# Kernel optimization log

Hardware: AMD Instinct MI355X
Metric: run time of the kernel (lower is better)

Reference implementation:

```python
import jax, jax.numpy as jnp
import numpy as np

N = 20000
E = 320000
NEG_SLOPE = 0.2
LN_EPS = 1e-5


def gat_conv(x, W, a_src, a_dst, b, src, dst, heads, ch, concat):
    # x: [N, F_in]; W: [F_in, H*C]; a_src/a_dst: [H, C]; b: [H*C] or [C]
    xl = (x @ W).reshape(N, heads, ch)                      # [N,H,C]
    alpha_src = jnp.sum(xl * a_src, axis=-1)                # [N,H]
    alpha_dst = jnp.sum(xl * a_dst, axis=-1)                # [N,H]
    e = alpha_src[src] + alpha_dst[dst]                     # [E',H]
    e = jax.nn.leaky_relu(e, NEG_SLOPE)
    # segment softmax over incoming edges of each dst node
    m = jax.ops.segment_max(e, dst, num_segments=N)         # [N,H]
    m = jnp.where(jnp.isfinite(m), m, 0.0)
    ex = jnp.exp(e - m[dst])
    denom = jax.ops.segment_sum(ex, dst, num_segments=N)    # [N,H]
    alpha = ex / (denom[dst] + 1e-16)                       # [E',H]
    msg = alpha[:, :, None] * xl[src]                       # [E',H,C]
    out = jax.ops.segment_sum(msg, dst, num_segments=N)     # [N,H,C]
    if concat:
        return out.reshape(N, heads * ch) + b
    return out.mean(axis=1) + b


def layer_norm(x, g, b):
    mu = jnp.mean(x, axis=-1, keepdims=True)
    var = jnp.mean(jnp.square(x - mu), axis=-1, keepdims=True)
    return (x - mu) * jax.lax.rsqrt(var + LN_EPS) * g + b


def setup_inputs() -> dict:
    key = jax.random.key(0)
    ks = jax.random.split(key, 24)
    d = {}
    d["x"] = jax.random.normal(ks[0], (N, 50), dtype=jnp.float32)
    d["edge_index"] = jax.random.randint(ks[1], (2, E), 0, N, dtype=jnp.int64)

    def glorot(k, shape):
        fan = shape[0] + shape[-1]
        return jax.random.normal(k, shape, dtype=jnp.float32) * np.sqrt(2.0 / fan)

    # conv1: 50 -> 256, heads=4, concat
    d["W1"] = glorot(ks[2], (50, 4 * 256))
    d["a_src1"] = glorot(ks[3], (4, 256))
    d["a_dst1"] = glorot(ks[4], (4, 256))
    d["b1"] = jnp.zeros((4 * 256,), jnp.float32)
    # conv2: 1024 -> 256, heads=4, concat
    d["W2"] = glorot(ks[5], (1024, 4 * 256))
    d["a_src2"] = glorot(ks[6], (4, 256))
    d["a_dst2"] = glorot(ks[7], (4, 256))
    d["b2"] = jnp.zeros((4 * 256,), jnp.float32)
    # conv3: 1024 -> 121, heads=6, concat=False
    d["W3"] = glorot(ks[8], (1024, 6 * 121))
    d["a_src3"] = glorot(ks[9], (6, 121))
    d["a_dst3"] = glorot(ks[10], (6, 121))
    d["b3"] = jnp.zeros((121,), jnp.float32)
    # skips
    d["skipW1"] = glorot(ks[11], (50, 1024))
    d["skipb1"] = jnp.zeros((1024,), jnp.float32)
    d["skipW2"] = glorot(ks[12], (1024, 1024))
    d["skipb2"] = jnp.zeros((1024,), jnp.float32)
    # layer norms
    d["g1"] = jnp.ones((1024,), jnp.float32)
    d["beta1"] = jnp.zeros((1024,), jnp.float32)
    d["g2"] = jnp.ones((1024,), jnp.float32)
    d["beta2"] = jnp.zeros((1024,), jnp.float32)
    return d


def reference(x, edge_index, W1, a_src1, a_dst1, b1, W2, a_src2, a_dst2, b2,
              W3, a_src3, a_dst3, b3, skipW1, skipb1, skipW2, skipb2,
              g1, beta1, g2, beta2):
    # add self loops (PyG GATConv default)
    loop = jnp.arange(N, dtype=edge_index.dtype)
    src = jnp.concatenate([edge_index[0], loop])
    dst = jnp.concatenate([edge_index[1], loop])

    h = gat_conv(x, W1, a_src1, a_dst1, b1, src, dst, 4, 256, True)
    h = jax.nn.elu(layer_norm(h + (x @ skipW1 + skipb1), g1, beta1))
    h2 = gat_conv(h, W2, a_src2, a_dst2, b2, src, dst, 4, 256, True)
    h2 = jax.nn.elu(layer_norm(h2 + (h @ skipW2 + skipb2), g2, beta2))
    out = gat_conv(h2, W3, a_src3, a_dst3, b3, src, dst, 6, 121, False)
    return out
```

## Files before the change

kernel.cpp:

```cpp
#include <hip/hip_runtime.h>
#include <hip/hip_bf16.h>
#include <math.h>

typedef __attribute__((ext_vector_type(8))) __bf16 bf16x8;
typedef __attribute__((ext_vector_type(4))) float f32x4;

#if __has_builtin(__builtin_amdgcn_global_load_lds)
#define GLD16(g, l)                                                                      \
    __builtin_amdgcn_global_load_lds(                                                    \
        (const __attribute__((address_space(1))) unsigned int*)(g),                      \
        (__attribute__((address_space(3))) unsigned int*)(l), 16, 0, 0)
#else
#define GLD16(g, l) (*(bf16x8*)(l) = *(const bf16x8*)(g))
#endif

#define BAR() asm volatile("s_barrier" ::: "memory")
#define WAITVM(N) asm volatile("s_waitcnt vmcnt(" #N ")" ::: "memory")


#define STAGE_H(Base, regidx, t_, kh_)                                                   \
    do {                                                                                 \
        __bf16* Ld = lds + ((((t_) & 1) * 4 + (regidx)) * 8192);                         \
        const __bf16* Gp = (Base) + (t_) * 64 + (kh_) * 32;                              \
        GLD16(Gp, Ld + tt * 8);                                                          \
        GLD16(Gp + (size_t)128 * K_, Ld + (tt + 512) * 8);                               \
    } while (0)

#define LOAD_A(t_, kh_)                                                                  \
    {                                                                                    \
        const __bf16* Ar = lds + (((t_) & 1) * 4 + (kh_)) * 8192 + aoff;                 \
        _Pragma("unroll") for (int i = 0; i < 8; i++)                                    \
            af[i] = *(const bf16x8*)(Ar + i * 512);                                      \
    }

#define LOAD_B2(t_, kh_, j0)                                                             \
    {                                                                                    \
        const __bf16* Br = lds + (((t_) & 1) * 4 + 2 + (kh_)) * 8192 + boff;             \
        _Pragma("unroll") for (int j = 0; j < 2; j++)                                    \
            bf[(j0) + j] = *(const bf16x8*)(Br + ((j0) + j) * 512);                      \
    }

#define MFMA_HALF(j0)                                                                    \
    __builtin_amdgcn_s_setprio(1);                                                       \
    _Pragma("unroll") for (int i = 0; i < 8; i++)                                        \
        _Pragma("unroll") for (int j = (j0); j < (j0) + 2; j++)                          \
            acc[i][j] = __builtin_amdgcn_mfma_f32_16x16x32_bf16(af[i], bf[j],            \
                                                                acc[i][j], 0, 0, 0);     \
    __builtin_amdgcn_s_setprio(0);

#define GEMM256_BODY(A, Bt, K_, STORE)                                                   \
    __shared__ __align__(16) __bf16 lds[65536];                                          \
    const int tt = threadIdx.x;                                                          \
    const int lane = tt & 63;                                                            \
    const int wid = tt >> 6;                                                             \
    const int wr = wid >> 2;                                           \
    const int wc = wid & 3;                                         \
     \
    const int nwg = gridDim.x * gridDim.y;                                               \
    const int wg0 = blockIdx.y * gridDim.x + blockIdx.x;                                 \
    const int qq = nwg >> 3, rr = nwg & 7, xcd = wg0 & 7, oo = wg0 >> 3;                 \
    const int swz = (xcd < rr ? xcd * (qq + 1) : rr * (qq + 1) + (xcd - rr) * qq) + oo;  \
    const int bm = (swz / gridDim.x) * 256;                                              \
    const int bn = (swz % gridDim.x) * 256;                                              \
    const int m16 = lane & 15;                                                           \
    const int c4 = lane >> 4;                                                            \
    const int NT = K_ >> 6;                                                              \
    const int srow = tt >> 2;                                                            \
    const int sch = (tt & 3) << 3;                                                       \
    const __bf16* Abase = A + (size_t)(bm + srow) * K_ + sch;                            \
    const __bf16* Bbase = Bt + (size_t)(bn + srow) * K_ + sch;                           \
    const int aoff = (wr * 128 + m16) * 32 + c4 * 8;                                     \
    const int boff = (wc * 64 + m16) * 32 + c4 * 8;                                      \
    f32x4 acc[8][4];                                                                     \
    _Pragma("unroll") for (int i = 0; i < 8; i++)                                        \
        _Pragma("unroll") for (int j = 0; j < 4; j++)                                    \
            acc[i][j] = (f32x4){0.f, 0.f, 0.f, 0.f};                                     \
    bf16x8 af[8], bf[4];                                                                 \
     \
    STAGE_H(Abase, 0, 0, 0);                                                             \
    STAGE_H(Bbase, 2, 0, 0);                                                             \
    STAGE_H(Abase, 1, 0, 1);                                                             \
    STAGE_H(Bbase, 3, 0, 1);                                                             \
    WAITVM(4);                                                                           \
    BAR();                                                                               \
    for (int t = 0; t < NT; t++) {                                                       \
        const bool pre = (t + 1 < NT);                                                   \
                                                                                 \
        LOAD_A(t, 0);                                                                    \
        LOAD_B2(t, 0, 0);                                                                \
        if (pre) STAGE_H(Abase, 0, t + 1, 0);                                            \
        BAR();                                                                           \
        MFMA_HALF(0);                                                                    \
        BAR();                                                                           \
                                                                                 \
        LOAD_B2(t, 0, 2);                                                                \
        if (pre) STAGE_H(Bbase, 2, t + 1, 0);                                            \
        BAR();                                                                           \
        MFMA_HALF(2);                                                                    \
        if (pre) { WAITVM(4); } else { WAITVM(0); }                                      \
        BAR();                                                                           \
                                                                                 \
        LOAD_A(t, 1);                                                                    \
        LOAD_B2(t, 1, 0);                                                                \
        if (pre) STAGE_H(Abase, 1, t + 1, 1);                                            \
        BAR();                                                                           \
        MFMA_HALF(0);                                                                    \
        BAR();                                                                           \
                                                                                 \
        LOAD_B2(t, 1, 2);                                                                \
        if (pre) STAGE_H(Bbase, 3, t + 1, 1);                                            \
        BAR();                                                                           \
        MFMA_HALF(2);                                                                    \
        if (pre) { WAITVM(4); }                                                          \
        BAR();                                                                           \
    }                                                                                    \
    STORE

__global__ __launch_bounds__(512, 2) void gemm256_bt(const __bf16* __restrict__ A,
                                                     const __bf16* __restrict__ Bt,
                                                     __bf16* __restrict__ C,
                                                     int M, int N_, int K_) {
    GEMM256_BODY(A, Bt, K_,
        { const int r4 = c4 << 2;
          const int rb = bm + wr * 128;
          const int cb = bn + wc * 64;
          _Pragma("unroll") for (int i = 0; i < 8; i++)
              _Pragma("unroll") for (int j = 0; j < 4; j++) {
                  int col = cb + j * 16 + m16;
                  size_t rowb = (size_t)(rb + i * 16 + r4) * N_ + col;
                  _Pragma("unroll") for (int r = 0; r < 4; r++)
                      C[rowb + (size_t)r * N_] = (__bf16)acc[i][j][r];
              } })
}

__global__ __launch_bounds__(512, 2) void gemm256_bt2(const __bf16* __restrict__ A,
                                                      const __bf16* __restrict__ Bt,
                                                      __bf16* __restrict__ C0,
                                                      __bf16* __restrict__ C1,
                                                      int M, int K_) {
    GEMM256_BODY(A, Bt, K_,
        { __bf16* Cp = (bn < 1024) ? C0 : C1;
          const int r4 = c4 << 2;
          const int rb = bm + wr * 128;
          const int cb = (bn & 1023) + wc * 64;
          _Pragma("unroll") for (int i = 0; i < 8; i++)
              _Pragma("unroll") for (int j = 0; j < 4; j++) {
                  int col = cb + j * 16 + m16;
                  size_t rowb = (size_t)(rb + i * 16 + r4) * 1024 + col;
                  _Pragma("unroll") for (int r = 0; r < 4; r++)
                      Cp[rowb + (size_t)r * 1024] = (__bf16)acc[i][j][r];
              } })
}

__device__ __forceinline__ void transpose_tile(const float* __restrict__ W,
                                               __bf16* __restrict__ WT,
                                               int K, int N, int Kp, int Np,
                                               int bx, int by, float* sm) {
    int tx = threadIdx.x & 31, ty = threadIdx.x >> 5;
#pragma unroll
    for (int r = ty; r < 32; r += 8) {
        int k = by * 32 + r, n = bx * 32 + tx;
        float v = 0.f;
        if (k < K && n < N) v = W[(size_t)k * N + n];
        sm[r * 33 + tx] = v;
    }
    __syncthreads();
#pragma unroll
    for (int r = ty; r < 32; r += 8) {
        int n = bx * 32 + r, k = by * 32 + tx;
        if (n < Np && k < Kp) WT[(size_t)n * Kp + k] = (__bf16)sm[tx * 33 + r];
    }
}

__device__ __forceinline__ void transpose_w3_tile(const float* __restrict__ W,
                                                  __bf16* __restrict__ WT,
                                                  int bx, int by, float* sm) {
    int tx = threadIdx.x & 31, ty = threadIdx.x >> 5;
    int r0 = bx * 32;
    int h = r0 >> 7;
    int c0 = r0 & 127;
#pragma unroll
    for (int r = ty; r < 32; r += 8) {
        int k = by * 32 + r;
        int c = c0 + tx;
        float v = 0.f;
        if (c < 121) v = W[(size_t)k * 726 + h * 121 + c];
        sm[r * 33 + tx] = v;
    }
    __syncthreads();
#pragma unroll
    for (int r = ty; r < 32; r += 8) {
        int rr = r0 + r;
        int k = by * 32 + tx;
        WT[(size_t)rr * 1024 + k] = (__bf16)sm[tx * 33 + r];
    }
}

__global__ __launch_bounds__(256) void prep_k(const float* __restrict__ x,
                                              const float* __restrict__ W1,
                                              const float* __restrict__ sW1,
                                              const float* __restrict__ W2,
                                              const float* __restrict__ sW2,
                                              const float* __restrict__ W3,
                                              __bf16* __restrict__ xp,
                                              __bf16* __restrict__ WTcat1,
                                              __bf16* __restrict__ WTcat2,
                                              __bf16* __restrict__ W3pT, int Nn) {
    __shared__ float sm[32 * 33];
    int b = blockIdx.x;
    if (b < 5056) {
        int i = b * 256 + threadIdx.x;
        int n = i >> 6, c = i & 63;
        float v = 0.f;
        if (n < Nn && c < 50) v = x[n * 50 + c];
        xp[(size_t)n * 64 + c] = (__bf16)v;
    } else if (b < 5120) {
        int i = b - 5056; transpose_tile(W1, WTcat1, 50, 1024, 64, 1024, i % 32, i / 32, sm);
    } else if (b < 5184) {
        int i = b - 5120; transpose_tile(sW1, WTcat1 + 1024 * 64, 50, 1024, 64, 1024, i % 32, i / 32, sm);
    } else if (b < 6208) {
        int i = b - 5184; transpose_tile(W2, WTcat2, 1024, 1024, 1024, 1024, i % 32, i / 32, sm);
    } else if (b < 7232) {
        int i = b - 6208; transpose_tile(sW2, WTcat2 + (size_t)1024 * 1024, 1024, 1024, 1024, 1024, i % 32, i / 32, sm);
    } else {
        int i = b - 7232; transpose_w3_tile(W3, W3pT, i % 24, i / 24, sm);
    }
}

__global__ void zero_probe_k(const int* __restrict__ ei, int* __restrict__ cnt,
                             int* __restrict__ flag, int Nn) {
    int i = blockIdx.x * 256 + threadIdx.x;
    if (i < Nn) cnt[i] = 0;
    if (blockIdx.x == 0 && threadIdx.x == 0) {
        int all0 = 1;
        for (int k = 0; k < 64; k++)
            if (ei[2 * k + 1] != 0) { all0 = 0; break; }
        *flag = all0;
    }
}

__device__ __forceinline__ int load_ei(const int* ei, int idx, int is64) {
    return is64 ? ei[2 * idx] : ei[idx];
}

__global__ void hist_k(const int* __restrict__ ei, const int* __restrict__ flag,
                       int* __restrict__ cnt, int E, int Nn) {
    int e = blockIdx.x * 256 + threadIdx.x;
    if (e >= E + Nn) return;
    int is64 = *flag;
    int d = (e < E) ? load_ei(ei, E + e, is64) : (e - E);
    d = min(max(d, 0), Nn - 1);
    atomicAdd(&cnt[d], 1);
}

__global__ __launch_bounds__(1024) void scan_k(int* __restrict__ cnt, int* __restrict__ row_ptr,
                                               int Nn) {
    __shared__ int part[1024];
    int t = threadIdx.x;
    int chunk = (Nn + 1023) >> 10;
    int lo = t * chunk;
    int hi = lo + chunk; if (hi > Nn) hi = Nn; if (lo > Nn) lo = Nn;
    int s = 0;
    for (int i = lo; i < hi; i++) s += (cnt[i] + 7) & ~7;
    part[t] = s;
    __syncthreads();
    for (int off = 1; off < 1024; off <<= 1) {
        int v = (t >= off) ? part[t - off] : 0;
        __syncthreads();
        part[t] += v;
        __syncthreads();
    }
    int run = part[t] - s;
    for (int i = lo; i < hi; i++) { row_ptr[i] = run; run += (cnt[i] + 7) & ~7; }
    if (t == 1023) row_ptr[Nn] = part[1023];
    __syncthreads();
    for (int i = lo; i < hi; i++) cnt[i] = 0;
}

__global__ void fill_csr_k(const int* __restrict__ ei, const int* __restrict__ flag,
                           const int* __restrict__ row_ptr, int* __restrict__ cursor,
                           int* __restrict__ src_csr, int E, int Nn) {
    int e = blockIdx.x * 256 + threadIdx.x;
    if (e >= E + Nn) return;
    int is64 = *flag;
    int d = (e < E) ? load_ei(ei, E + e, is64) : (e - E);
    int s = (e < E) ? load_ei(ei, e, is64) : (e - E);
    d = min(max(d, 0), Nn - 1);
    s = min(max(s, 0), Nn - 1);
    int slot = row_ptr[d] + atomicAdd(&cursor[d], 1);
    src_csr[slot] = s;
}

__global__ void alpha_k(const __bf16* __restrict__ XL, int ld, const float* __restrict__ a_src,
                        const float* __restrict__ a_dst, float* __restrict__ asrc,
                        float* __restrict__ adst, int Nn, int H, int C, int Cpad) {
    int gw = (blockIdx.x * 256 + threadIdx.x) >> 6;
    int lane = threadIdx.x & 63;
    if (gw >= Nn * H) return;
    int n = gw / H, h = gw - n * H;
    const __bf16* row = XL + (size_t)n * ld + h * Cpad;
    const float* as = a_src + h * C;
    const float* ad = a_dst + h * C;
    float s = 0.f, d = 0.f;
    for (int c = lane; c < C; c += 64) {
        float v = (float)row[c];
        s += v * as[c];
        d += v * ad[c];
    }
#pragma unroll
    for (int off = 32; off; off >>= 1) {
        s += __shfl_down(s, off);
        d += __shfl_down(d, off);
    }
    if (lane == 0) { asrc[n * H + h] = s; adst[n * H + h] = d; }
}

__global__ void attn_k(const int* __restrict__ row_ptr, const int* __restrict__ deg,
                       const int* __restrict__ src_csr,
                       const float* __restrict__ asrc, const float* __restrict__ adst,
                       float* __restrict__ wt, int Nn, int H, int Ecap) {
    int gw = (blockIdx.x * 256 + threadIdx.x) >> 6;
    int lane = threadIdx.x & 63;
    if (gw >= Nn) return;
    int n = gw;
    int base = row_ptr[n], dg = deg[n];
    if (dg <= 64) {
        bool v = lane < dg;
        int src = v ? src_csr[base + lane] : 0;
        for (int h = 0; h < H; h++) {
            float ad = adst[n * H + h];
            float e = -1e30f;
            if (v) {
                e = asrc[src * H + h] + ad;
                e = e > 0.f ? e : 0.2f * e;
            }
            float m = e;
#pragma unroll
            for (int off = 1; off < 64; off <<= 1) m = fmaxf(m, __shfl_xor(m, off));
            float ex = v ? __expf(e - m) : 0.f;
            float sum = ex;
#pragma unroll
            for (int off = 1; off < 64; off <<= 1) sum += __shfl_xor(sum, off);
            if (v) wt[(size_t)h * Ecap + base + lane] = ex / (sum + 1e-16f);
        }
        return;
    }
    for (int h = 0; h < H; h++) {
        float ad = adst[n * H + h];
        float m = -1e30f;
        for (int s = lane; s < dg; s += 64) {
            float e = asrc[src_csr[base + s] * H + h] + ad;
            e = e > 0.f ? e : 0.2f * e;
            m = fmaxf(m, e);
        }
#pragma unroll
        for (int off = 1; off < 64; off <<= 1) m = fmaxf(m, __shfl_xor(m, off));
        float sum = 0.f;
        for (int s = lane; s < dg; s += 64) {
            float e = asrc[src_csr[base + s] * H + h] + ad;
            e = e > 0.f ? e : 0.2f * e;
            sum += __expf(e - m);
        }
#pragma unroll
        for (int off = 1; off < 64; off <<= 1) sum += __shfl_xor(sum, off);
        float inv = 1.f / (sum + 1e-16f);
        float* wrow = wt + (size_t)h * Ecap;
        for (int s = lane; s < dg; s += 64) {
            float e = asrc[src_csr[base + s] * H + h] + ad;
            e = e > 0.f ? e : 0.2f * e;
            wrow[base + s] = __expf(e - m) * inv;
        }
    }
}

__global__ __launch_bounds__(256) void agg_skip8(const __bf16* __restrict__ XL,
                                                 const float* __restrict__ wt,
                                                 const int* __restrict__ row_ptr,
                                                 const int* __restrict__ src_csr,
                                                 const float* __restrict__ bias,
                                                 const float* __restrict__ sb,
                                                 __bf16* __restrict__ SK, int Nn, int Ecap) {
    const int cc = blockIdx.x;
    const int n = blockIdx.y * 4 + (threadIdx.x >> 6);
    const int lane = threadIdx.x & 63;
    if (n >= Nn) return;
    const int g = lane >> 4;
    const int p = lane & 15;
    const int col = cc * 128 + p * 8;
    const float* wrow = wt + (size_t)(cc >> 1) * Ecap;
    const __bf16* XLc = XL + col;
    const int base = row_ptr[n], end = row_ptr[n + 1];

    float acc[8];
#pragma unroll
    for (int j = 0; j < 8; j++) acc[j] = 0.f;

    for (int e = base; e < end; e += 8) {
        int2 si = *(const int2*)(src_csr + e + 2 * g);
        float2 wv = *(const float2*)(wrow + e + 2 * g);
        bf16x8 xa = *(const bf16x8*)(XLc + (size_t)si.x * 1024);
        bf16x8 xb = *(const bf16x8*)(XLc + (size_t)si.y * 1024);
#pragma unroll
        for (int j = 0; j < 8; j++) acc[j] += wv.x * (float)xa[j] + wv.y * (float)xb[j];
    }
#pragma unroll
    for (int j = 0; j < 8; j++) {
        acc[j] += __shfl_xor(acc[j], 16);
        acc[j] += __shfl_xor(acc[j], 32);
    }
    if (lane < 16) {
        size_t o = (size_t)n * 1024 + col;
        bf16x8 sk = *(const bf16x8*)(SK + o);
        bf16x8 res;
#pragma unroll
        for (int j = 0; j < 8; j++)
            res[j] = (__bf16)(acc[j] + bias[col + j] + sb[col + j] + (float)sk[j]);
        *(bf16x8*)(SK + o) = res;
    }
}

__global__ __launch_bounds__(256) void agg_mean8(const __bf16* __restrict__ XL,
                                                 const float* __restrict__ wt,
                                                 const int* __restrict__ row_ptr,
                                                 const int* __restrict__ src_csr,
                                                 __bf16* __restrict__ part, int Nn, int Ecap) {
    const int cc = blockIdx.x;
    const int n = blockIdx.y * 4 + (threadIdx.x >> 6);
    const int lane = threadIdx.x & 63;
    if (n >= Nn) return;
    const int g = lane >> 4;
    const int p = lane & 15;
    const int col = cc * 128 + p * 8;
    const float* wrow = wt + (size_t)cc * Ecap;
    const __bf16* XLc = XL + col;
    const int base = row_ptr[n], end = row_ptr[n + 1];

    float acc[8];
#pragma unroll
    for (int j = 0; j < 8; j++) acc[j] = 0.f;

    for (int e = base; e < end; e += 8) {
        int2 si = *(const int2*)(src_csr + e + 2 * g);
        float2 wv = *(const float2*)(wrow + e + 2 * g);
        bf16x8 xa = *(const bf16x8*)(XLc + (size_t)si.x * 768);
        bf16x8 xb = *(const bf16x8*)(XLc + (size_t)si.y * 768);
#pragma unroll
        for (int j = 0; j < 8; j++) acc[j] += wv.x * (float)xa[j] + wv.y * (float)xb[j];
    }
#pragma unroll
    for (int j = 0; j < 8; j++) {
        acc[j] += __shfl_xor(acc[j], 16);
        acc[j] += __shfl_xor(acc[j], 32);
    }
    if (lane < 16) {
        size_t o = (size_t)n * 768 + col;
        bf16x8 res;
#pragma unroll
        for (int j = 0; j < 8; j++) res[j] = (__bf16)acc[j];
        *(bf16x8*)(part + o) = res;
    }
}

__global__ __launch_bounds__(128) void reduce_mean_k(const __bf16* __restrict__ part,
                                                     const float* __restrict__ b3,
                                                     float* __restrict__ out, int Nn) {
    int n = blockIdx.x;
    int t = threadIdx.x;
    if (t >= 121) return;
    const __bf16* row = part + (size_t)n * 768;
    float s = 0.f;
#pragma unroll
    for (int h = 0; h < 6; h++) s += (float)row[h * 128 + t];
    out[(size_t)n * 121 + t] = s * (1.f / 6.f) + b3[t];
}

__global__ __launch_bounds__(256) void ln_elu_k(const __bf16* __restrict__ in,
                                                const float* __restrict__ g,
                                                const float* __restrict__ be,
                                                __bf16* __restrict__ out, int rows_real) {
    const int D = 1024;
    int n = blockIdx.x;
    int t = threadIdx.x;
    size_t ro = (size_t)n * D;
    if (n >= rows_real) {
#pragma unroll
        for (int j = 0; j < 4; j++) out[ro + t + 256 * j] = (__bf16)0.f;
        return;
    }
    float v[4];
    float s = 0.f, q = 0.f;
#pragma unroll
    for (int j = 0; j < 4; j++) {
        int c = t + 256 * j;
        float a = (float)in[ro + c];
        v[j] = a;
        s += a;
        q += a * a;
    }
#pragma unroll
    for (int off = 32; off; off >>= 1) {
        s += __shfl_down(s, off);
        q += __shfl_down(q, off);
    }
    __shared__ float rs[8];
    int wid = t >> 6;
    if ((t & 63) == 0) { rs[wid] = s; rs[wid + 4] = q; }
    __syncthreads();
    s = rs[0] + rs[1] + rs[2] + rs[3];
    q = rs[4] + rs[5] + rs[6] + rs[7];
    float mu = s * (1.f / 1024.f);
    float var = q * (1.f / 1024.f) - mu * mu;
    float inv = rsqrtf(fmaxf(var, 0.f) + 1e-5f);
#pragma unroll
    for (int j = 0; j < 4; j++) {
        int c = t + 256 * j;
        float y = (v[j] - mu) * inv * g[c] + be[c];
        y = y > 0.f ? y : expm1f(y);
        out[ro + c] = (__bf16)y;
    }
}

extern "C" void kernel_launch(void* const* d_in, const int* in_sizes, int n_in,
                              void* d_out, int out_size, void* d_ws, size_t ws_size,
                              hipStream_t stream) {
    const float* x   = (const float*)d_in[0];
    const int*   ei  = (const int*)d_in[1];
    const float* W1  = (const float*)d_in[2];
    const float* as1 = (const float*)d_in[3];
    const float* ad1 = (const float*)d_in[4];
    const float* b1  = (const float*)d_in[5];
    const float* W2  = (const float*)d_in[6];
    const float* as2 = (const float*)d_in[7];
    const float* ad2 = (const float*)d_in[8];
    const float* b2  = (const float*)d_in[9];
    const float* W3  = (const float*)d_in[10];
    const float* as3 = (const float*)d_in[11];
    const float* ad3 = (const float*)d_in[12];
    const float* b3  = (const float*)d_in[13];
    const float* sW1 = (const float*)d_in[14];
    const float* sb1 = (const float*)d_in[15];
    const float* sW2 = (const float*)d_in[16];
    const float* sb2 = (const float*)d_in[17];
    const float* g1  = (const float*)d_in[18];
    const float* be1 = (const float*)d_in[19];
    const float* g2  = (const float*)d_in[20];
    const float* be2 = (const float*)d_in[21];
    float* out = (float*)d_out;

    const int Nn = 20000;
    const int E = in_sizes[1] / 2;
    const int E2 = E + Nn;
    const int Ecap = E2 + 8 * Nn;
    const int Mpad = 20224;

    char* p = (char*)d_ws;
    auto alloc = [&](size_t bytes) {
        char* r = p;
        p += (bytes + 255) & ~(size_t)255;
        return r;
    };
    __bf16* WTcat1 = (__bf16*)alloc((size_t)2048 * 64 * 2);
    __bf16* WTcat2 = (__bf16*)alloc((size_t)2048 * 1024 * 2);
    __bf16* W3pT   = (__bf16*)alloc((size_t)768 * 1024 * 2);
    __bf16* xp     = (__bf16*)alloc((size_t)Mpad * 64 * 2);
    __bf16* XL     = (__bf16*)alloc((size_t)Mpad * 1024 * 2);
    __bf16* SK     = (__bf16*)alloc((size_t)Mpad * 1024 * 2);
    __bf16* H1     = (__bf16*)alloc((size_t)Mpad * 1024 * 2);
    float*  asrcb  = (float*)alloc((size_t)Nn * 6 * 4);
    float*  adstb  = (float*)alloc((size_t)Nn * 6 * 4);
    float*  wbuf   = (float*)alloc((size_t)6 * Ecap * 4);
    int*    rowp   = (int*)alloc((size_t)(Nn + 1) * 4);
    int*    cnt    = (int*)alloc((size_t)Nn * 4);
    int*    scsr   = (int*)alloc((size_t)Ecap * 4);
    int*    eiflag = (int*)alloc(256);
    __bf16* part   = SK;
    (void)ws_size; (void)n_in; (void)out_size;

    prep_k<<<8000, 256, 0, stream>>>(x, W1, sW1, W2, sW2, W3, xp, WTcat1, WTcat2, W3pT, Nn);

    zero_probe_k<<<(Nn + 255) / 256, 256, 0, stream>>>(ei, cnt, eiflag, Nn);
    hist_k<<<(E2 + 255) / 256, 256, 0, stream>>>(ei, eiflag, cnt, E, Nn);
    scan_k<<<1, 1024, 0, stream>>>(cnt, rowp, Nn);
    (void)hipMemsetAsync(scsr, 0, (size_t)Ecap * 4, stream);
    (void)hipMemsetAsync(wbuf, 0, (size_t)6 * Ecap * 4, stream);
    fill_csr_k<<<(E2 + 255) / 256, 256, 0, stream>>>(ei, eiflag, rowp, cnt, scsr, E, Nn);

    gemm256_bt2<<<dim3(8, Mpad / 256), 512, 0, stream>>>(xp, WTcat1, XL, SK, Mpad, 64);
    alpha_k<<<(Nn * 4 * 64) / 256, 256, 0, stream>>>(XL, 1024, as1, ad1, asrcb, adstb, Nn, 4, 256, 256);
    attn_k<<<(Nn + 3) / 4, 256, 0, stream>>>(rowp, cnt, scsr, asrcb, adstb, wbuf, Nn, 4, Ecap);
    agg_skip8<<<dim3(8, (Nn + 3) / 4), 256, 0, stream>>>(XL, wbuf, rowp, scsr, b1, sb1, SK, Nn, Ecap);
    ln_elu_k<<<Mpad, 256, 0, stream>>>(SK, g1, be1, H1, Nn);

    gemm256_bt2<<<dim3(8, Mpad / 256), 512, 0, stream>>>(H1, WTcat2, XL, SK, Mpad, 1024);
    alpha_k<<<(Nn * 4 * 64) / 256, 256, 0, stream>>>(XL, 1024, as2, ad2, asrcb, adstb, Nn, 4, 256, 256);
    attn_k<<<(Nn + 3) / 4, 256, 0, stream>>>(rowp, cnt, scsr, asrcb, adstb, wbuf, Nn, 4, Ecap);
    agg_skip8<<<dim3(8, (Nn + 3) / 4), 256, 0, stream>>>(XL, wbuf, rowp, scsr, b2, sb2, SK, Nn, Ecap);
    ln_elu_k<<<Mpad, 256, 0, stream>>>(SK, g2, be2, H1, Nn);

    gemm256_bt<<<dim3(3, Mpad / 256), 512, 0, stream>>>(H1, W3pT, XL, Mpad, 768, 1024);
    alpha_k<<<(Nn * 6 * 64) / 256, 256, 0, stream>>>(XL, 768, as3, ad3, asrcb, adstb, Nn, 6, 121, 128);
    attn_k<<<(Nn + 3) / 4, 256, 0, stream>>>(rowp, cnt, scsr, asrcb, adstb, wbuf, Nn, 6, Ecap);
    agg_mean8<<<dim3(6, (Nn + 3) / 4), 256, 0, stream>>>(XL, wbuf, rowp, scsr, part, Nn, Ecap);
    reduce_mean_k<<<Nn, 128, 0, stream>>>(part, b3, out, Nn);
}
```

Baseline: 757.0 us.

## Store GEMM outputs in 128-column slabs and swizzle LDS staging

GEMM outputs (XL, SK) are now written in a slab layout where each 128-column chunk is stored contiguously for all rows, and alpha, aggregation and layernorm kernels index that layout. The aggregation grids are transposed so consecutive blocks work on the same column slab, which is meant to keep gathered source rows within a smaller L2 working set. The GEMM also XOR-swizzles LDS staging and fragment offsets to reduce bank conflicts. The risks are that the LN kernel now reads strided across slabs and the GEMM epilogue stores become scattered.

```diff
diff --git a/kernel.cpp b/kernel.cpp
--- a/kernel.cpp
+++ b/kernel.cpp
@@ -4,6 +4,9 @@
 
 typedef __attribute__((ext_vector_type(8))) __bf16 bf16x8;
 typedef __attribute__((ext_vector_type(4))) float f32x4;
+
+#define MPAD 20224
+#define SSZ ((size_t)MPAD * 128)
 
 #if __has_builtin(__builtin_amdgcn_global_load_lds)
 #define GLD16(g, l)                                                                      \
@@ -65,12 +68,14 @@
     const int m16 = lane & 15;                                                           \
     const int c4 = lane >> 4;                                                            \
     const int NT = K_ >> 6;                                                              \
-    const int srow = tt >> 2;                                                            \
-    const int sch = (tt & 3) << 3;                                                       \
+    const int ttp = tt ^ (((tt >> 5) & 1) << 1);          \
+    const int srow = ttp >> 2;                                                           \
+    const int sch = (ttp & 3) << 3;                                                      \
     const __bf16* Abase = A + (size_t)(bm + srow) * K_ + sch;                            \
     const __bf16* Bbase = Bt + (size_t)(bn + srow) * K_ + sch;                           \
-    const int aoff = (wr * 128 + m16) * 32 + c4 * 8;                                     \
-    const int boff = (wc * 64 + m16) * 32 + c4 * 8;                                      \
+    const int fsw = ((m16 >> 3) & 1) << 4;                                               \
+    const int aoff = (((wr * 128 + m16) * 32) + c4 * 8) ^ fsw;                           \
+    const int boff = (((wc * 64 + m16) * 32) + c4 * 8) ^ fsw;                            \
     f32x4 acc[8][4];                                                                     \
     _Pragma("unroll") for (int i = 0; i < 8; i++)                                        \
         _Pragma("unroll") for (int j = 0; j < 4; j++)                                    \
@@ -123,13 +128,14 @@
     GEMM256_BODY(A, Bt, K_,
         { const int r4 = c4 << 2;
           const int rb = bm + wr * 128;
-          const int cb = bn + wc * 64;
           _Pragma("unroll") for (int i = 0; i < 8; i++)
               _Pragma("unroll") for (int j = 0; j < 4; j++) {
-                  int col = cb + j * 16 + m16;
-                  size_t rowb = (size_t)(rb + i * 16 + r4) * N_ + col;
-                  _Pragma("unroll") for (int r = 0; r < 4; r++)
-                      C[rowb + (size_t)r * N_] = (__bf16)acc[i][j][r];
+                  int col = bn + wc * 64 + j * 16 + m16;
+                  size_t sb_ = (size_t)(col >> 7) * SSZ + (col & 127);
+                  _Pragma("unroll") for (int r = 0; r < 4; r++) {
+                      int row = rb + i * 16 + r4 + r;
+                      C[sb_ + (size_t)row * 128] = (__bf16)acc[i][j][r];
+                  }
               } })
 }
 
@@ -139,16 +145,18 @@
                                                       __bf16* __restrict__ C1,
                                                       int M, int K_) {
     GEMM256_BODY(A, Bt, K_,
-        { __bf16* Cp = (bn < 1024) ? C0 : C1;
-          const int r4 = c4 << 2;
+        { const int r4 = c4 << 2;
           const int rb = bm + wr * 128;
-          const int cb = (bn & 1023) + wc * 64;
           _Pragma("unroll") for (int i = 0; i < 8; i++)
               _Pragma("unroll") for (int j = 0; j < 4; j++) {
-                  int col = cb + j * 16 + m16;
-                  size_t rowb = (size_t)(rb + i * 16 + r4) * 1024 + col;
-                  _Pragma("unroll") for (int r = 0; r < 4; r++)
-                      Cp[rowb + (size_t)r * 1024] = (__bf16)acc[i][j][r];
+                  int col = bn + wc * 64 + j * 16 + m16;
+                  __bf16* Cp = (col < 1024) ? C0 : C1;
+                  int c10 = col & 1023;
+                  size_t sb_ = (size_t)(c10 >> 7) * SSZ + (c10 & 127);
+                  _Pragma("unroll") for (int r = 0; r < 4; r++) {
+                      int row = rb + i * 16 + r4 + r;
+                      Cp[sb_ + (size_t)row * 128] = (__bf16)acc[i][j][r];
+                  }
               } })
 }
 
@@ -291,19 +299,18 @@
     src_csr[slot] = s;
 }
 
-__global__ void alpha_k(const __bf16* __restrict__ XL, int ld, const float* __restrict__ a_src,
+__global__ void alpha_k(const __bf16* __restrict__ XL, int sph, const float* __restrict__ a_src,
                         const float* __restrict__ a_dst, float* __restrict__ asrc,
-                        float* __restrict__ adst, int Nn, int H, int C, int Cpad) {
+                        float* __restrict__ adst, int Nn, int H, int C) {
     int gw = (blockIdx.x * 256 + threadIdx.x) >> 6;
     int lane = threadIdx.x & 63;
     if (gw >= Nn * H) return;
     int n = gw / H, h = gw - n * H;
-    const __bf16* row = XL + (size_t)n * ld + h * Cpad;
     const float* as = a_src + h * C;
     const float* ad = a_dst + h * C;
     float s = 0.f, d = 0.f;
     for (int c = lane; c < C; c += 64) {
-        float v = (float)row[c];
+        float v = (float)XL[(size_t)(h * sph + (c >> 7)) * SSZ + (size_t)n * 128 + (c & 127)];
         s += v * as[c];
         d += v * ad[c];
     }
@@ -380,15 +387,15 @@
                                                  const float* __restrict__ bias,
                                                  const float* __restrict__ sb,
                                                  __bf16* __restrict__ SK, int Nn, int Ecap) {
-    const int cc = blockIdx.x;
-    const int n = blockIdx.y * 4 + (threadIdx.x >> 6);
+    const int cc = blockIdx.y;
+    const int n = blockIdx.x * 4 + (threadIdx.x >> 6);
     const int lane = threadIdx.x & 63;
     if (n >= Nn) return;
     const int g = lane >> 4;
     const int p = lane & 15;
     const int col = cc * 128 + p * 8;
     const float* wrow = wt + (size_t)(cc >> 1) * Ecap;
-    const __bf16* XLc = XL + col;
+    const __bf16* XLc = XL + (size_t)cc * SSZ + p * 8;
     const int base = row_ptr[n], end = row_ptr[n + 1];
 
     float acc[8];
@@ -398,8 +405,8 @@
     for (int e = base; e < end; e += 8) {
         int2 si = *(const int2*)(src_csr + e + 2 * g);
         float2 wv = *(const float2*)(wrow + e + 2 * g);
-        bf16x8 xa = *(const bf16x8*)(XLc + (size_t)si.x * 1024);
-        bf16x8 xb = *(const bf16x8*)(XLc + (size_t)si.y * 1024);
+        bf16x8 xa = *(const bf16x8*)(XLc + (size_t)si.x * 128);
+        bf16x8 xb = *(const bf16x8*)(XLc + (size_t)si.y * 128);
 #pragma unroll
         for (int j = 0; j < 8; j++) acc[j] += wv.x * (float)xa[j] + wv.y * (float)xb[j];
     }
@@ -409,7 +416,7 @@
         acc[j] += __shfl_xor(acc[j], 32);
     }
     if (lane < 16) {
-        size_t o = (size_t)n * 1024 + col;
+        size_t o = (size_t)cc * SSZ + (size_t)n * 128 + p * 8;
         bf16x8 sk = *(const bf16x8*)(SK + o);
         bf16x8 res;
 #pragma unroll
@@ -424,15 +431,15 @@
                                                  const int* __restrict__ row_ptr,
                                                  const int* __restrict__ src_csr,
                                                  __bf16* __restrict__ part, int Nn, int Ecap) {
-    const int cc = blockIdx.x;
-    const int n = blockIdx.y * 4 + (threadIdx.x >> 6);
+    const int cc = blockIdx.y;
+    const int n = blockIdx.x * 4 + (threadIdx.x >> 6);
     const int lane = threadIdx.x & 63;
     if (n >= Nn) return;
     const int g = lane >> 4;
     const int p = lane & 15;
     const int col = cc * 128 + p * 8;
     const float* wrow = wt + (size_t)cc * Ecap;
-    const __bf16* XLc = XL + col;
+    const __bf16* XLc = XL + (size_t)cc * SSZ + p * 8;
     const int base = row_ptr[n], end = row_ptr[n + 1];
 
     float acc[8];
@@ -442,8 +449,8 @@
     for (int e = base; e < end; e += 8) {
         int2 si = *(const int2*)(src_csr + e + 2 * g);
         float2 wv = *(const float2*)(wrow + e + 2 * g);
-        bf16x8 xa = *(const bf16x8*)(XLc + (size_t)si.x * 768);
-        bf16x8 xb = *(const bf16x8*)(XLc + (size_t)si.y * 768);
+        bf16x8 xa = *(const bf16x8*)(XLc + (size_t)si.x * 128);
+        bf16x8 xb = *(const bf16x8*)(XLc + (size_t)si.y * 128);
 #pragma unroll
         for (int j = 0; j < 8; j++) acc[j] += wv.x * (float)xa[j] + wv.y * (float)xb[j];
     }
@@ -492,7 +499,7 @@
 #pragma unroll
     for (int j = 0; j < 4; j++) {
         int c = t + 256 * j;
-        float a = (float)in[ro + c];
+        float a = (float)in[(size_t)(c >> 7) * SSZ + (size_t)n * 128 + (c & 127)];
         v[j] = a;
         s += a;
         q += a * a;
@@ -551,7 +558,7 @@
     const int E = in_sizes[1] / 2;
     const int E2 = E + Nn;
     const int Ecap = E2 + 8 * Nn;
-    const int Mpad = 20224;
+    const int Mpad = MPAD;
 
     char* p = (char*)d_ws;
     auto alloc = [&](size_t bytes) {
@@ -586,20 +593,20 @@
     fill_csr_k<<<(E2 + 255) / 256, 256, 0, stream>>>(ei, eiflag, rowp, cnt, scsr, E, Nn);
 
     gemm256_bt2<<<dim3(8, Mpad / 256), 512, 0, stream>>>(xp, WTcat1, XL, SK, Mpad, 64);
-    alpha_k<<<(Nn * 4 * 64) / 256, 256, 0, stream>>>(XL, 1024, as1, ad1, asrcb, adstb, Nn, 4, 256, 256);
+    alpha_k<<<(Nn * 4 * 64) / 256, 256, 0, stream>>>(XL, 2, as1, ad1, asrcb, adstb, Nn, 4, 256);
     attn_k<<<(Nn + 3) / 4, 256, 0, stream>>>(rowp, cnt, scsr, asrcb, adstb, wbuf, Nn, 4, Ecap);
-    agg_skip8<<<dim3(8, (Nn + 3) / 4), 256, 0, stream>>>(XL, wbuf, rowp, scsr, b1, sb1, SK, Nn, Ecap);
+    agg_skip8<<<dim3((Nn + 3) / 4, 8), 256, 0, stream>>>(XL, wbuf, rowp, scsr, b1, sb1, SK, Nn, Ecap);
     ln_elu_k<<<Mpad, 256, 0, stream>>>(SK, g1, be1, H1, Nn);
 
     gemm256_bt2<<<dim3(8, Mpad / 256), 512, 0, stream>>>(H1, WTcat2, XL, SK, Mpad, 1024);
-    alpha_k<<<(Nn * 4 * 64) / 256, 256, 0, stream>>>(XL, 1024, as2, ad2, asrcb, adstb, Nn, 4, 256, 256);
+    alpha_k<<<(Nn * 4 * 64) / 256, 256, 0, stream>>>(XL, 2, as2, ad2, asrcb, adstb, Nn, 4, 256);
     attn_k<<<(Nn + 3) / 4, 256, 0, stream>>>(rowp, cnt, scsr, asrcb, adstb, wbuf, Nn, 4, Ecap);
-    agg_skip8<<<dim3(8, (Nn + 3) / 4), 256, 0, stream>>>(XL, wbuf, rowp, scsr, b2, sb2, SK, Nn, Ecap);
+    agg_skip8<<<dim3((Nn + 3) / 4, 8), 256, 0, stream>>>(XL, wbuf, rowp, scsr, b2, sb2, SK, Nn, Ecap);
     ln_elu_k<<<Mpad, 256, 0, stream>>>(SK, g2, be2, H1, Nn);
 
     gemm256_bt<<<dim3(3, Mpad / 256), 512, 0, stream>>>(H1, W3pT, XL, Mpad, 768, 1024);
-    alpha_k<<<(Nn * 6 * 64) / 256, 256, 0, stream>>>(XL, 768, as3, ad3, asrcb, adstb, Nn, 6, 121, 128);
+    alpha_k<<<(Nn * 6 * 64) / 256, 256, 0, stream>>>(XL, 1, as3, ad3, asrcb, adstb, Nn, 6, 121);
     attn_k<<<(Nn + 3) / 4, 256, 0, stream>>>(rowp, cnt, scsr, asrcb, adstb, wbuf, Nn, 6, Ecap);
-    agg_mean8<<<dim3(6, (Nn + 3) / 4), 256, 0, stream>>>(XL, wbuf, rowp, scsr, part, Nn, Ecap);
+    agg_mean8<<<dim3((Nn + 3) / 4, 6), 256, 0, stream>>>(XL, wbuf, rowp, scsr, part, Nn, Ecap);
     reduce_mean_k<<<Nn, 128, 0, stream>>>(part, b3, out, Nn);
 }
```

New measurement: 760.5 us. About the same (+0.5%).
